# Kernel optimization log

Measured on AMD Instinct MI355X. Metric: run time of the kernel, lower is better.

The kernel has to match this reference:

```python
import jax, jax.numpy as jnp
import numpy as np


def setup_inputs() -> dict:
    key = jax.random.key(0)
    k1, k2, k3, k4, k5 = jax.random.split(key, 5)
    N, IN, OUT, E = 100000, 512, 256, 3200000
    x = jax.random.normal(k1, (N, IN), dtype=jnp.float32)
    # xavier-uniform init for weight
    limit = float(np.sqrt(6.0 / (IN + OUT)))
    weight = jax.random.uniform(k2, (IN, OUT), dtype=jnp.float32, minval=-limit, maxval=limit)
    edge_rows = jax.random.randint(k3, (E,), 0, N, dtype=jnp.int32)
    edge_cols = jax.random.randint(k4, (E,), 0, N, dtype=jnp.int32)
    edge_vals = jax.random.uniform(k5, (E,), dtype=jnp.float32)
    return {"x": x, "weight": weight, "edge_rows": edge_rows,
            "edge_cols": edge_cols, "edge_vals": edge_vals, "active": 1}


def reference(x, weight, edge_rows, edge_cols, edge_vals, active):
    N = x.shape[0]
    # dense matmul (+ optional tanh)
    support = x @ weight  # [N, OUT]
    if active:
        support = jnp.tanh(support)
    # spmm(adj, support): out[r] = sum_e vals[e] * support[cols[e]] for rows[e]==r
    gathered = support[edge_cols] * edge_vals[:, None]  # [E, OUT]
    out = jax.ops.segment_sum(gathered, edge_rows, num_segments=N)
    return out
```

## Files before the change

### kernel.cpp

```cpp
#include <hip/hip_runtime.h>
#include <hip/hip_bf16.h>

#define IN_DIM  512
#define OUT_DIM 256

#define RPB     64
#define MAXNB   1600
#define BCAP    2432
#define SCHUNK  12800

using bf16x8 = __attribute__((ext_vector_type(8))) __bf16;
using f32x4  = __attribute__((ext_vector_type(4))) float;

__device__ __forceinline__ void async_lds16(const void* g, void* l) {
    __builtin_amdgcn_global_load_lds(
        (const __attribute__((address_space(1))) void*)g,
        (__attribute__((address_space(3))) void*)l, 16, 0, 0);
}

__global__ void convert_weight(const float* __restrict__ W, __bf16* __restrict__ Wt) {
    int idx = blockIdx.x * blockDim.x + threadIdx.x;
    int n = idx >> 9;
    int k = idx & 511;
    Wt[idx] = (__bf16)W[k * OUT_DIM + n];
}

__launch_bounds__(256)
__global__ void gemm_tanh(const float* __restrict__ x, const __bf16* __restrict__ Wt,
                          __hip_bfloat16* __restrict__ support, const int* __restrict__ active,
                          int N) {
    __shared__ __bf16 Bt[2][256 * 32];

    const int tid  = threadIdx.x;
    const int wave = tid >> 6;
    const int lane = tid & 63;
    const int m    = lane & 15;
    const int quad = lane >> 4;

    int r0 = blockIdx.x * 64 + wave * 16;
    if (r0 + 16 > N) r0 = N - 16;

    const float* xrow = x + (size_t)(r0 + m) * IN_DIM;

    const char* WtB = (const char*)Wt;

    f32x4 acc[16];
#pragma unroll
    for (int t = 0; t < 16; ++t) acc[t] = (f32x4)0.0f;

    {
        const int k0 = 0;
#pragma unroll
        for (int j = 0; j < 4; ++j) {
            int idx = j * 256 + tid;
            int n = idx >> 2, kp = idx & 3;
            async_lds16(WtB + (size_t)n * 1024 + k0 * 2 + kp * 16,
                        (char*)&Bt[0][0] + ((j * 4 + wave) * 64 + lane) * 16);
        }
    }

    int cur = 0;
    for (int kk = 0; kk < 16; ++kk) {
        __syncthreads();
        if (kk + 1 < 16) {
            const int k0n = (kk + 1) * 32;
#pragma unroll
            for (int j = 0; j < 4; ++j) {
                int idx = j * 256 + tid;
                int n = idx >> 2, kp = idx & 3;
                async_lds16(WtB + (size_t)n * 1024 + k0n * 2 + kp * 16,
                            (char*)&Bt[cur ^ 1][0] + ((j * 4 + wave) * 64 + lane) * 16);
            }
        }

        const float4* ap = (const float4*)(xrow + kk * 32 + quad * 8);
        float4 a0 = ap[0];
        float4 a1 = ap[1];
        bf16x8 af;
        af[0] = (__bf16)a0.x; af[1] = (__bf16)a0.y; af[2] = (__bf16)a0.z; af[3] = (__bf16)a0.w;
        af[4] = (__bf16)a1.x; af[5] = (__bf16)a1.y; af[6] = (__bf16)a1.z; af[7] = (__bf16)a1.w;

#pragma unroll
        for (int t = 0; t < 16; ++t) {
            bf16x8 bf = *(const bf16x8*)&Bt[cur][(t * 16 + m) * 32 + quad * 8];
            acc[t] = __builtin_amdgcn_mfma_f32_16x16x32_bf16(af, bf, acc[t], 0, 0, 0);
        }
        cur ^= 1;
    }

    const int act = active[0];
    const int row_base = r0 + quad * 4;
#pragma unroll
    for (int t = 0; t < 16; ++t) {
#pragma unroll
        for (int r = 0; r < 4; ++r) {
            float v = acc[t][r];
            if (act) v = tanhf(v);
            support[(size_t)(row_base + r) * OUT_DIM + t * 16 + m] = __float2bfloat16(v);
        }
    }
}

__launch_bounds__(512)
__global__ void bucket_scatter(const int* __restrict__ rows, const int* __restrict__ cols,
                               const float* __restrict__ vals, int* __restrict__ gcur,
                               unsigned long long* __restrict__ sorted, int E, int nb) {
    __shared__ unsigned long long buf[SCHUNK];
    __shared__ int cnt[MAXNB];
    __shared__ int lbase[MAXNB];
    __shared__ int lcur[MAXNB];
    __shared__ int gbase_s[MAXNB];

    const int tid = threadIdx.x;
    const int e0  = blockIdx.x * SCHUNK;
    const int n   = min(SCHUNK, E - e0);

    for (int i = tid; i < nb; i += 512) cnt[i] = 0;
    __syncthreads();

    for (int i = tid; i < n; i += 512)
        atomicAdd(&cnt[rows[e0 + i] >> 6], 1);
    __syncthreads();

    if (tid < 64) {
        int carry = 0;
        for (int base_i = 0; base_i < nb; base_i += 64) {
            int i = base_i + tid;
            int v = (i < nb) ? cnt[i] : 0;
            int pref = v;
#pragma unroll
            for (int d = 1; d < 64; d <<= 1) {
                int up = __shfl_up(pref, d, 64);
                if (tid >= d) pref += up;
            }
            if (i < nb) { lbase[i] = carry + pref - v; lcur[i] = carry + pref - v; }
            carry += __shfl(pref, 63, 64);
        }
    }
    __syncthreads();

    for (int i = tid; i < n; i += 512) {
        int r = rows[e0 + i];
        int b = r >> 6;
        unsigned int low = (unsigned int)cols[e0 + i] | (((unsigned int)(r & 63)) << 17);
        unsigned long long packed = (unsigned long long)low |
            ((unsigned long long)(unsigned int)__float_as_int(vals[e0 + i]) << 32);
        int pos = atomicAdd(&lcur[b], 1);
        buf[pos] = packed;
    }
    __syncthreads();

    for (int b = tid; b < nb; b += 512) {
        int c = cnt[b];
        gbase_s[b] = c ? atomicAdd(&gcur[b], c) : 0;
    }
    __syncthreads();

    const int qw = tid >> 4, ln = tid & 15;
    for (int b = qw; b < nb; b += 32) {
        int c = cnt[b];
        if (c == 0) continue;
        int gb = gbase_s[b];
        int lim = BCAP - gb;
        if (c > lim) c = (lim > 0) ? lim : 0;
        int src = lbase[b];
        unsigned long long* dst = sorted + (size_t)b * BCAP + gb;
        for (int j = ln; j < c; j += 16) dst[j] = buf[src + j];
    }
}

__launch_bounds__(256)
__global__ void bucket_accumulate(const unsigned short* __restrict__ support,
                                  const int* __restrict__ gcur,
                                  const unsigned long long* __restrict__ sorted,
                                  float* __restrict__ out, int N) {
    __shared__ unsigned long long seg[BCAP];
    __shared__ int rcnt[RPB];
    __shared__ int rbase[RPB];
    __shared__ int rcur[RPB];

    const int b   = blockIdx.x;
    const int tid = threadIdx.x;
    const int r0  = b * RPB;

    int scnt = gcur[b];
    if (scnt > BCAP) scnt = BCAP;
    const size_t s0 = (size_t)b * BCAP;

    if (tid < RPB) rcnt[tid] = 0;
    __syncthreads();

    for (int i = tid; i < scnt; i += 256)
        atomicAdd(&rcnt[(int)((sorted[s0 + i] >> 17) & 63)], 1);
    __syncthreads();

    if (tid < 64) {
        int v = rcnt[tid];
        int pref = v;
#pragma unroll
        for (int d = 1; d < 64; d <<= 1) {
            int up = __shfl_up(pref, d, 64);
            if (tid >= d) pref += up;
        }
        rbase[tid] = pref - v;
        rcur[tid]  = pref - v;
    }
    __syncthreads();

    for (int i = tid; i < scnt; i += 256) {
        unsigned long long p = sorted[s0 + i];
        int rib = (int)((p >> 17) & 63);
        int pos = atomicAdd(&rcur[rib], 1);
        seg[pos] = p;
    }
    __syncthreads();

    const int wave = tid >> 6, lane = tid & 63;
    const uint2* supb = (const uint2*)support;
    for (int k = 0; k < 16; ++k) {
        int rib = wave * 16 + k;
        int r = r0 + rib;
        if (r >= N) break;
        int e   = rbase[rib];
        int end = e + rcnt[rib];

        float a0 = 0.f, a1 = 0.f, a2 = 0.f, a3 = 0.f;

        for (; e + 8 <= end; e += 8) {
            unsigned long long pp[8];
#pragma unroll
            for (int j = 0; j < 8; ++j) pp[j] = seg[e + j];
            uint2 uu[8];
#pragma unroll
            for (int j = 0; j < 8; ++j) {
                int c = (int)(pp[j] & 0x1FFFF);
                uu[j] = supb[((size_t)c << 6) + lane];
            }
#pragma unroll
            for (int j = 0; j < 8; ++j) {
                float v = __uint_as_float((unsigned int)(pp[j] >> 32));
                a0 = fmaf(v, __uint_as_float(uu[j].x << 16),          a0);
                a1 = fmaf(v, __uint_as_float(uu[j].x & 0xffff0000u),  a1);
                a2 = fmaf(v, __uint_as_float(uu[j].y << 16),          a2);
                a3 = fmaf(v, __uint_as_float(uu[j].y & 0xffff0000u),  a3);
            }
        }
        for (; e + 4 <= end; e += 4) {
            unsigned long long pp[4];
#pragma unroll
            for (int j = 0; j < 4; ++j) pp[j] = seg[e + j];
            uint2 uu[4];
#pragma unroll
            for (int j = 0; j < 4; ++j) {
                int c = (int)(pp[j] & 0x1FFFF);
                uu[j] = supb[((size_t)c << 6) + lane];
            }
#pragma unroll
            for (int j = 0; j < 4; ++j) {
                float v = __uint_as_float((unsigned int)(pp[j] >> 32));
                a0 = fmaf(v, __uint_as_float(uu[j].x << 16),          a0);
                a1 = fmaf(v, __uint_as_float(uu[j].x & 0xffff0000u),  a1);
                a2 = fmaf(v, __uint_as_float(uu[j].y << 16),          a2);
                a3 = fmaf(v, __uint_as_float(uu[j].y & 0xffff0000u),  a3);
            }
        }
        for (; e < end; ++e) {
            unsigned long long p = seg[e];
            int   c = (int)(p & 0x1FFFF);
            float v = __uint_as_float((unsigned int)(p >> 32));
            uint2 u = supb[((size_t)c << 6) + lane];
            a0 = fmaf(v, __uint_as_float(u.x << 16),          a0);
            a1 = fmaf(v, __uint_as_float(u.x & 0xffff0000u),  a1);
            a2 = fmaf(v, __uint_as_float(u.y << 16),          a2);
            a3 = fmaf(v, __uint_as_float(u.y & 0xffff0000u),  a3);
        }
        float4 o;
        o.x = a0; o.y = a1; o.z = a2; o.w = a3;
        *((float4*)(out + (size_t)r * OUT_DIM) + lane) = o;
    }
}

extern "C" void kernel_launch(void* const* d_in, const int* in_sizes, int n_in,
                              void* d_out, int out_size, void* d_ws, size_t ws_size,
                              hipStream_t stream) {
    const float* x     = (const float*)d_in[0];
    const float* W     = (const float*)d_in[1];
    const int*   erows = (const int*)d_in[2];
    const int*   ecols = (const int*)d_in[3];
    const float* evals = (const float*)d_in[4];
    const int*   activ = (const int*)d_in[5];
    float*       out   = (float*)d_out;

    const int N = in_sizes[0] / IN_DIM;
    const int E = in_sizes[2];
    const int nb = (N + RPB - 1) / RPB;

    char* p = (char*)d_ws;
    unsigned short* support = (unsigned short*)p;  p += (size_t)N * OUT_DIM * sizeof(unsigned short);
    __bf16* Wt      = (__bf16*)p;           p += (size_t)IN_DIM * OUT_DIM * sizeof(__bf16);
    int*    gcur    = (int*)p;              p += ((size_t)nb * sizeof(int) + 15) & ~(size_t)15;
    unsigned long long* sorted = (unsigned long long*)p;  p += (size_t)nb * BCAP * sizeof(unsigned long long);

    convert_weight<<<(IN_DIM * OUT_DIM) / 256, 256, 0, stream>>>(W, Wt);

    const int gemm_blocks = (N + 63) / 64;
    gemm_tanh<<<gemm_blocks, 256, 0, stream>>>(x, Wt, (__hip_bfloat16*)support, activ, N);

    hipMemsetAsync(gcur, 0, (size_t)nb * sizeof(int), stream);

    const int sblocks = (E + SCHUNK - 1) / SCHUNK;
    bucket_scatter<<<sblocks, 512, 0, stream>>>(erows, ecols, evals, gcur, sorted, E, nb);

    bucket_accumulate<<<nb, 256, 0, stream>>>(support, gcur, sorted, out, N);
}
```

Measured before the change: 658.8 us.

## Sort bucket edges by row and column slice to improve gather locality

In the accumulate kernel, edges are now counting-sorted on a composite key of row plus a 32-way column slice taken from bits of the column index, rather than on row alone. Within each row the gathers of support rows then follow column order, which should give better L2/TLB locality. The output store becomes a nontemporal store, and the scatter chunk size is halved so more scatter blocks are launched. In exchange the block uses a 2048-entry LDS histogram and a longer serial scan done by a single wave.

```diff
diff --git a/kernel.cpp b/kernel.cpp
--- a/kernel.cpp
+++ b/kernel.cpp
@@ -7,7 +7,8 @@
 #define RPB     64
 #define MAXNB   1600
 #define BCAP    2432
-#define SCHUNK  12800
+#define SCHUNK  6400
+#define NSL     32
 
 using bf16x8 = __attribute__((ext_vector_type(8))) __bf16;
 using f32x4  = __attribute__((ext_vector_type(4))) float;
@@ -175,9 +176,9 @@
                                   const unsigned long long* __restrict__ sorted,
                                   float* __restrict__ out, int N) {
     __shared__ unsigned long long seg[BCAP];
-    __shared__ int rcnt[RPB];
-    __shared__ int rbase[RPB];
-    __shared__ int rcur[RPB];
+    __shared__ int kcnt[RPB * NSL];
+    __shared__ int kbase[RPB * NSL];
+    __shared__ int rowstart[RPB + 1];
 
     const int b   = blockIdx.x;
     const int tid = threadIdx.x;
@@ -187,30 +188,41 @@
     if (scnt > BCAP) scnt = BCAP;
     const size_t s0 = (size_t)b * BCAP;
 
-    if (tid < RPB) rcnt[tid] = 0;
-    __syncthreads();
-
-    for (int i = tid; i < scnt; i += 256)
-        atomicAdd(&rcnt[(int)((sorted[s0 + i] >> 17) & 63)], 1);
-    __syncthreads();
-
-    if (tid < 64) {
-        int v = rcnt[tid];
-        int pref = v;
-#pragma unroll
-        for (int d = 1; d < 64; d <<= 1) {
-            int up = __shfl_up(pref, d, 64);
-            if (tid >= d) pref += up;
-        }
-        rbase[tid] = pref - v;
-        rcur[tid]  = pref - v;
-    }
+    for (int i = tid; i < RPB * NSL; i += 256) kcnt[i] = 0;
     __syncthreads();
 
     for (int i = tid; i < scnt; i += 256) {
         unsigned long long p = sorted[s0 + i];
-        int rib = (int)((p >> 17) & 63);
-        int pos = atomicAdd(&rcur[rib], 1);
+        int key = (int)(((p >> 17) & 63) << 5) | (int)((p >> 12) & 31);
+        atomicAdd(&kcnt[key], 1);
+    }
+    __syncthreads();
+
+    if (tid < 64) {
+        int carry = 0;
+        for (int ch = 0; ch < RPB * NSL; ch += 64) {
+            int i = ch + tid;
+            int v = kcnt[i];
+            int pref = v;
+#pragma unroll
+            for (int d = 1; d < 64; d <<= 1) {
+                int up = __shfl_up(pref, d, 64);
+                if (tid >= d) pref += up;
+            }
+            kbase[i] = carry + pref - v;
+            carry += __shfl(pref, 63, 64);
+        }
+    }
+    __syncthreads();
+
+    if (tid < RPB) rowstart[tid] = kbase[tid << 5];
+    if (tid == 0)  rowstart[RPB] = scnt;
+    __syncthreads();
+
+    for (int i = tid; i < scnt; i += 256) {
+        unsigned long long p = sorted[s0 + i];
+        int key = (int)(((p >> 17) & 63) << 5) | (int)((p >> 12) & 31);
+        int pos = atomicAdd(&kbase[key], 1);
         seg[pos] = p;
     }
     __syncthreads();
@@ -221,8 +233,8 @@
         int rib = wave * 16 + k;
         int r = r0 + rib;
         if (r >= N) break;
-        int e   = rbase[rib];
-        int end = e + rcnt[rib];
+        int e   = rowstart[rib];
+        int end = rowstart[rib + 1];
 
         float a0 = 0.f, a1 = 0.f, a2 = 0.f, a3 = 0.f;
 
@@ -274,9 +286,9 @@
             a2 = fmaf(v, __uint_as_float(u.y << 16),          a2);
             a3 = fmaf(v, __uint_as_float(u.y & 0xffff0000u),  a3);
         }
-        float4 o;
-        o.x = a0; o.y = a1; o.z = a2; o.w = a3;
-        *((float4*)(out + (size_t)r * OUT_DIM) + lane) = o;
+        f32x4 o;
+        o[0] = a0; o[1] = a1; o[2] = a2; o[3] = a3;
+        __builtin_nontemporal_store(o, (f32x4*)(out + (size_t)r * OUT_DIM) + lane);
     }
 }
 
@@ -306,7 +318,7 @@
     const int gemm_blocks = (N + 63) / 64;
     gemm_tanh<<<gemm_blocks, 256, 0, stream>>>(x, Wt, (__hip_bfloat16*)support, activ, N);
 
-    hipMemsetAsync(gcur, 0, (size_t)nb * sizeof(int), stream);
+    (void)hipMemsetAsync(gcur, 0, (size_t)nb * sizeof(int), stream);
 
     const int sblocks = (E + SCHUNK - 1) / SCHUNK;
     bucket_scatter<<<sblocks, 512, 0, stream>>>(erows, ecols, evals, gcur, sorted, E, nb);
```

New measurement: 650.9 us. About the same (-1.2%).
